# Optimization experiments

Measured on AMD Instinct MI355X. Metric: run time of the kernel, lower is better.

## Reference

```python
import jax, jax.numpy as jnp
import numpy as np

K = -1.0          # manifold curvature (hyperbolic / Poincare ball)
SK = 1.0          # sqrt(|K|)
EPS = 1e-7


def _artan_k(x):
    # inverse of tan_k for K<0: artanh(sqrt(|K|) x)/sqrt(|K|)
    return jnp.arctanh(jnp.clip(SK * x, -1.0 + EPS, 1.0 - EPS)) / SK


def _tan_k(x):
    return jnp.tanh(SK * x) / SK


def _norm(x):
    return jnp.maximum(jnp.linalg.norm(x, axis=-1, keepdims=True), 1e-15)


def mobius_add(x, y):
    xy = jnp.sum(x * y, -1, keepdims=True)
    x2 = jnp.sum(x * x, -1, keepdims=True)
    y2 = jnp.sum(y * y, -1, keepdims=True)
    num = (1.0 - 2.0 * K * xy - K * y2) * x + (1.0 + K * x2) * y
    den = 1.0 - 2.0 * K * xy + K * K * x2 * y2
    return num / jnp.maximum(den, 1e-15)


def mobius_scalar_mul(r, x):
    # r may be scalar or (n,1) per-row scalar
    xn = _norm(x)
    return _tan_k(r * _artan_k(xn)) * x / xn


def mobius_matvec(W, x):
    # geoopt convention: (m @ x) per point -> x @ W^T
    xn = _norm(x)
    mx = x @ W.T
    mxn = _norm(mx)
    return _tan_k(mxn / xn * _artan_k(xn)) * mx / mxn


def lambda_x(x):
    # conformal factor lambda_x = 2 / (1 + K |x|^2); returns shape (...,)
    return 2.0 / jnp.maximum(1.0 + K * jnp.sum(x * x, -1), 1e-10)


def expmap0(u):
    un = _norm(u)
    return _tan_k(un) * u / un


def logmap0(y):
    yn = _norm(y)
    return _artan_k(yn) * y / yn


def kappa_left_multiply(A, X):
    # Vectorized per-node weighted gyro-midpoint + mobius scalar mul.
    # out_i = (sum_j A_ij) otimes gyromidpoint(X, weights=A_i)
    gamma = lambda_x(X)                              # (n,)
    denom = A @ (gamma - 1.0)                        # (n,)
    denom = jnp.where(jnp.abs(denom) < 1e-10, 1e-10, denom)
    nom = A @ (gamma[:, None] * X)                   # (n,d)
    two_mean = nom / denom[:, None]
    m = mobius_scalar_mul(0.5, two_mean)             # gyromidpoint
    return mobius_scalar_mul(jnp.sum(A, axis=1, keepdims=True), m)


def setup_inputs() -> dict:
    key = jax.random.key(0)
    k1, k2, k3, k4, k5 = jax.random.split(key, 5)
    n, d, c = 8192, 256, 16
    # node embeddings on the Poincare ball (small norm, well inside the ball)
    X = 0.01 * jax.random.normal(k1, (n, d), jnp.float32)
    # dense normalized adjacency (positive weights, row sums O(1))
    A_hat = jax.random.uniform(k2, (n, n), dtype=jnp.float32) / n
    W = jax.random.uniform(k3, (d, d), dtype=jnp.float32)        # torch.rand init
    W_logits = jax.random.uniform(k4, (d, c), dtype=jnp.float32)
    # p_ks = expmap0(rand), scaled for numerical stability
    p_ks = expmap0(0.05 * jax.random.uniform(k5, (c, d), dtype=jnp.float32))
    return {"X": X, "A_hat": A_hat, "W": W, "W_logits": W_logits, "p_ks": p_ks}


def reference(X, A_hat, W, W_logits, p_ks):
    # hidden kappa-GCN layer
    XW = mobius_matvec(W, X)                          # (n,d)
    AXW = kappa_left_multiply(A_hat, XW)              # (n,d)
    H1 = expmap0(jax.nn.relu(logmap0(AXW)))           # manifold.apply(relu)
    # hyperbolic logits (kappa != 0 branch, K<0 -> asinh)
    z = mobius_add(-p_ks[None, :, :], H1[:, None, :]) # (n,k,d)
    z_n = jnp.linalg.norm(z, axis=-1)                 # (n,k)
    a_n = jnp.maximum(jnp.linalg.norm(W_logits, axis=0), 1e-15)  # (k,)
    za = jnp.einsum('nkd,dk->nk', z, W_logits)
    den = jnp.maximum(1.0 + K * z_n * z_n, 1e-10) * a_n
    dist = jnp.arcsinh(2.0 * SK * za / den)
    lam = lambda_x(p_ks)                              # (k,)
    logits = (lam * a_n / SK) * dist                  # (n,k)
    return A_hat @ logits
```

## Files before the change

kernel.cpp:

```cpp
#include <hip/hip_runtime.h>
#include <math.h>

#define Nn 8192
#define Dd 256
#define Cc 16

#define OFF_BP   4194304u
#define OFF_G1B  5373952u
#define OFF_DEN  5378048u
#define OFF_RS   5410816u
#define OFF_KC   5443584u
#define OFF_LB   5443648u
#define WS_FLOATS 5509184u

typedef short vshort8 __attribute__((ext_vector_type(8)));
typedef float vfloat4 __attribute__((ext_vector_type(4)));

#define AS1 __attribute__((address_space(1)))
#define AS3 __attribute__((address_space(3)))

__device__ __forceinline__ float clip1(float x) {
    return fminf(fmaxf(x, -1.0f + 1e-7f), 1.0f - 1e-7f);
}

__device__ __forceinline__ unsigned short f2bf(float f) {
    unsigned int u = __float_as_uint(f);
    u += 0x7fff + ((u >> 16) & 1);
    return (unsigned short)(u >> 16);
}

__device__ __forceinline__ float bf2f(unsigned short b) {
    return __uint_as_float(((unsigned int)b) << 16);
}

__device__ __forceinline__ float waveReduce(float v) {
    #pragma unroll
    for (int off = 32; off; off >>= 1) v += __shfl_down(v, off);
    return v;
}

__device__ __forceinline__ float blockReduceBcast(float v, float* red) {
    int t = threadIdx.x, w = t >> 6, l = t & 63;
    v = waveReduce(v);
    if (l == 0) red[w] = v;
    __syncthreads();
    if (t == 0) red[0] = red[0] + red[1] + red[2] + red[3];
    __syncthreads();
    float r = red[0];
    __syncthreads();
    return r;
}

__global__ __launch_bounds__(256) void k_front(const float* __restrict__ X,
                                               const float* __restrict__ W,
                                               const float* __restrict__ Wl,
                                               const float* __restrict__ Pk,
                                               unsigned short* __restrict__ Bp,
                                               unsigned short* __restrict__ g1b,
                                               float* __restrict__ kc) {
    __shared__ __align__(16) unsigned short Xs[32][256];
    __shared__ __align__(16) unsigned short Gs[32][258];
    __shared__ float xs2[32];
    __shared__ float scal[32];
    __shared__ float red4[32][4];

    const int t = threadIdx.x;

    if (blockIdx.x >= 256) {
        int k = blockIdx.x - 256;
        float* red = &red4[0][0];
        float pv = Pk[k * Dd + t];
        float wv = Wl[t * Cc + k];
        float p2 = blockReduceBcast(pv * pv, red);
        float pw = blockReduceBcast(pv * wv, red);
        float w2 = blockReduceBcast(wv * wv, red);
        if (t == 0) {
            float an  = fmaxf(sqrtf(w2), 1e-15f);
            float lam = 2.0f / fmaxf(1.0f - p2, 1e-10f);
            kc[k * 4 + 0] = p2; kc[k * 4 + 1] = pw;
            kc[k * 4 + 2] = an; kc[k * 4 + 3] = lam;
        }
        return;
    }

    const int l = t & 63, w = t >> 6;
    const int ll = l & 15, kh = l >> 4;
    const int m0 = blockIdx.x * 32;
    const int ar = t >> 3, aq = t & 7;
    const int c0 = w * 64;

    float x2p = 0.f;
    #pragma unroll
    for (int tc = 0; tc < 4; ++tc) {
        const float* xp = &X[(size_t)(m0 + ar) * Dd + tc * 64 + aq * 8];
        vfloat4 v0 = *(const vfloat4*)xp;
        vfloat4 v1 = *(const vfloat4*)(xp + 4);
        vshort8 o;
        #pragma unroll
        for (int e = 0; e < 4; ++e) {
            x2p += v0[e] * v0[e] + v1[e] * v1[e];
            o[e] = (short)f2bf(v0[e]);
            o[e + 4] = (short)f2bf(v1[e]);
        }
        int byte = (tc * 64 + aq * 8) * 2;
        *(vshort8*)((char*)&Xs[ar][0] + (byte ^ ((ar & 7) << 4))) = o;
    }
    x2p += __shfl_xor(x2p, 1); x2p += __shfl_xor(x2p, 2); x2p += __shfl_xor(x2p, 4);
    if (aq == 0) xs2[ar] = x2p;
    __syncthreads();

    vfloat4 acc[2][4];
    #pragma unroll
    for (int mi = 0; mi < 2; ++mi)
        #pragma unroll
        for (int ni = 0; ni < 4; ++ni)
            acc[mi][ni] = (vfloat4){0.f, 0.f, 0.f, 0.f};
    #pragma unroll
    for (int tc = 0; tc < 4; ++tc) {
        vshort8 bf[8];
        #pragma unroll
        for (int ni = 0; ni < 4; ++ni)
            #pragma unroll
            for (int kk = 0; kk < 2; ++kk) {
                const float* wp = &W[(size_t)(c0 + ni * 16 + ll) * Dd
                                     + tc * 64 + kh * 8 + kk * 32];
                vfloat4 b0 = *(const vfloat4*)wp;
                vfloat4 b1 = *(const vfloat4*)(wp + 4);
                vshort8 o;
                #pragma unroll
                for (int e = 0; e < 4; ++e) {
                    o[e] = (short)f2bf(b0[e]);
                    o[e + 4] = (short)f2bf(b1[e]);
                }
                bf[ni * 2 + kk] = o;
            }
        #pragma unroll
        for (int kk = 0; kk < 2; ++kk) {
            int byte = (tc * 64 + kh * 8 + kk * 32) * 2;
            vshort8 af[2];
            #pragma unroll
            for (int mi = 0; mi < 2; ++mi) {
                int row = mi * 16 + ll;
                af[mi] = *(const vshort8*)((const char*)&Xs[row][0]
                                           + (byte ^ ((row & 7) << 4)));
            }
            #pragma unroll
            for (int mi = 0; mi < 2; ++mi)
                #pragma unroll
                for (int ni = 0; ni < 4; ++ni)
                    acc[mi][ni] = __builtin_amdgcn_mfma_f32_16x16x32_bf16(
                        af[mi], bf[ni * 2 + kk], acc[mi][ni], 0, 0, 0);
        }
    }

    #pragma unroll
    for (int mi = 0; mi < 2; ++mi)
        #pragma unroll
        for (int j = 0; j < 4; ++j) {
            float p = 0.f;
            #pragma unroll
            for (int ni = 0; ni < 4; ++ni)
                p += acc[mi][ni][j] * acc[mi][ni][j];
            p += __shfl_xor(p, 1); p += __shfl_xor(p, 2);
            p += __shfl_xor(p, 4); p += __shfl_xor(p, 8);
            if (ll == 0) red4[mi * 16 + kh * 4 + j][w] = p;
        }
    __syncthreads();

    if (t < 32) {
        float mx2 = red4[t][0] + red4[t][1] + red4[t][2] + red4[t][3];
        float xn = fmaxf(sqrtf(xs2[t]), 1e-15f);
        float mxn = fmaxf(sqrtf(mx2), 1e-15f);
        float s = tanhf(mxn / xn * atanhf(clip1(xn))) / mxn;
        float xw2 = s * s * mx2;
        float gamma = 2.0f / fmaxf(1.0f - xw2, 1e-10f);
        scal[t] = gamma * s;
        g1b[m0 + t] = f2bf(gamma - 1.0f);
    }
    __syncthreads();

    #pragma unroll
    for (int mi = 0; mi < 2; ++mi)
        #pragma unroll
        for (int ni = 0; ni < 4; ++ni) {
            int row = mi * 16 + kh * 4;
            int col = c0 + ni * 16 + ll;
            #pragma unroll
            for (int j = 0; j < 4; ++j)
                Gs[row + j][col] = f2bf(scal[row + j] * acc[mi][ni][j]);
        }
    __syncthreads();

    const int s = blockIdx.x;
    #pragma unroll
    for (int pass = 0; pass < 4; ++pass) {
        int c = pass * 256 + t;
        int gni = c >> 6, lc = c & 63;
        int col = (gni >> 2) * 64 + (gni & 3) * 16 + (lc & 15);
        int kh8 = (lc >> 4) * 8;
        vshort8 o;
        #pragma unroll
        for (int e = 0; e < 8; ++e) o[e] = (short)Gs[kh8 + e][col];
        *(vshort8*)&Bp[((size_t)(s * 16 + gni) * 64 + lc) * 8] = o;
    }
}

__device__ __forceinline__ void g2_issueB(const unsigned short* __restrict__ Bp,
        unsigned short (&BsB)[16][512], int splt, int slab, int w, int l) {
    #pragma unroll
    for (int ni = 0; ni < 4; ++ni)
        __builtin_amdgcn_global_load_lds(
            (const AS1 unsigned int*)
                (Bp + ((size_t)((splt * 64 + slab) * 16 + w * 4 + ni) * 512) + l * 8),
            (AS3 unsigned int*)&BsB[w * 4 + ni][0], 16, 0, 0);
}

__device__ __forceinline__ void g2_loadA(const float* __restrict__ Abase,
                                         int tile, float (&a8)[8]) {
    const vfloat4* p = (const vfloat4*)(Abase + tile * 32);
    *(vfloat4*)&a8[0] = p[0];
    *(vfloat4*)&a8[4] = p[1];
}

__device__ __forceinline__ void g2_stage(unsigned short (&AsB)[2048],
        const unsigned short* g1s, const float (&a8)[8],
        int tile, int rowst, int kq, float& dacc, float& racc) {
    vshort8 gv = *(const vshort8*)&g1s[tile * 32 + kq * 8];
    vshort8 o;
    #pragma unroll
    for (int e = 0; e < 8; ++e) {
        float av = a8[e];
        o[e] = (short)f2bf(av);
        dacc += av * bf2f((unsigned short)gv[e]);
        racc += av;
    }
    *(vshort8*)((char*)&AsB[0] + rowst * 64 + ((kq * 16) ^ ((rowst & 3) << 4))) = o;
}

__device__ __forceinline__ void g2_mfma(const unsigned short (&AsB)[2048],
        const unsigned short (&BsB)[16][512], int w, int kh, int ll15, int l,
        vfloat4 (&acc)[4][4]) {
    vshort8 bf[4], af[4];
    #pragma unroll
    for (int ni = 0; ni < 4; ++ni)
        bf[ni] = *(const vshort8*)&BsB[w * 4 + ni][l * 8];
    #pragma unroll
    for (int mi = 0; mi < 4; ++mi) {
        int row = mi * 16 + ll15;
        af[mi] = *(const vshort8*)((const char*)&AsB[0]
                  + row * 64 + ((kh * 16) ^ ((row & 3) << 4)));
    }
    __builtin_amdgcn_s_setprio(1);
    #pragma unroll
    for (int mi = 0; mi < 4; ++mi)
        #pragma unroll
        for (int ni = 0; ni < 4; ++ni)
            acc[mi][ni] = __builtin_amdgcn_mfma_f32_16x16x32_bf16(
                af[mi], bf[ni], acc[mi][ni], 0, 0, 0);
    __builtin_amdgcn_s_setprio(0);
}

__global__ __launch_bounds__(256, 2) void k_gemm1_mfma(
        const float* __restrict__ A,
        const unsigned short* __restrict__ Bp,
        const unsigned short* __restrict__ g1b,
        unsigned short* __restrict__ Pp,
        float* __restrict__ denp,
        float* __restrict__ rsp) {
    __shared__ __align__(16) unsigned short As[2][2048];
    __shared__ __align__(16) unsigned short Bs[4][16][512];
    __shared__ __align__(16) unsigned short g1s[2048];

    const int t = threadIdx.x, l = t & 63, w = t >> 6;
    const int id = blockIdx.x;
    const int splt = id & 3;
    const int m0 = (id >> 2) * 64;
    const int kb = splt * 2048;
    const int kh = l >> 4, ll15 = l & 15;
    const int rowst = t >> 2, kq = t & 3;

    const float* Abase = &A[(size_t)(m0 + rowst) * Nn + kb + kq * 8];

    vfloat4 acc[4][4];
    #pragma unroll
    for (int mi = 0; mi < 4; ++mi)
        #pragma unroll
        for (int ni = 0; ni < 4; ++ni)
            acc[mi][ni] = (vfloat4){0.f, 0.f, 0.f, 0.f};
    float dacc = 0.f, racc = 0.f;
    float a0[8], a1[8], a2[8], a3[8];

    uint4 g1v = *(const uint4*)&g1b[kb + t * 8];
    g2_issueB(Bp, Bs[0], splt, 0, w, l);
    g2_issueB(Bp, Bs[1], splt, 1, w, l);
    g2_issueB(Bp, Bs[2], splt, 2, w, l);
    g2_loadA(Abase, 0, a0);
    g2_loadA(Abase, 1, a1);
    g2_loadA(Abase, 2, a2);
    g2_loadA(Abase, 3, a3);
    asm volatile("s_waitcnt vmcnt(0)" ::: "memory");
    *(uint4*)&g1s[t * 8] = g1v;
    asm volatile("s_waitcnt lgkmcnt(0)" ::: "memory");
    __builtin_amdgcn_s_barrier();
    g2_stage(As[0], g1s, a0, 0, rowst, kq, dacc, racc);
    asm volatile("s_waitcnt lgkmcnt(0)" ::: "memory");
    __builtin_amdgcn_s_barrier();
    __builtin_amdgcn_sched_barrier(0);

    for (int u = 0; u < 16; ++u) {
        #pragma unroll
        for (int pp = 0; pp < 4; ++pp) {
            const int q = u * 4 + pp;
            g2_issueB(Bp, Bs[(pp + 3) & 3], splt, (q + 3) & 63, w, l);
            {
                float (&adst)[8] = (pp == 0) ? a0 : (pp == 1) ? a1
                                 : (pp == 2) ? a2 : a3;
                g2_loadA(Abase, (q + 4) & 63, adst);
            }
            asm volatile("s_waitcnt vmcnt(18)" ::: "memory");
            if (q < 63) {
                float (&asrc)[8] = (pp == 0) ? a1 : (pp == 1) ? a2
                                 : (pp == 2) ? a3 : a0;
                g2_stage(As[(q + 1) & 1], g1s, asrc, q + 1, rowst, kq, dacc, racc);
            }
            g2_mfma(As[q & 1], Bs[pp & 3], w, kh, ll15, l, acc);
            asm volatile("s_waitcnt lgkmcnt(0)" ::: "memory");
            __builtin_amdgcn_s_barrier();
            __builtin_amdgcn_sched_barrier(0);
        }
    }

    dacc += __shfl_xor(dacc, 1); dacc += __shfl_xor(dacc, 2);
    racc += __shfl_xor(racc, 1); racc += __shfl_xor(racc, 2);
    if (kq == 0) {
        denp[splt * Nn + m0 + rowst] = dacc;
        rsp [splt * Nn + m0 + rowst] = racc;
    }

    unsigned short* P = Pp + (size_t)splt * ((size_t)Nn * Dd);
    #pragma unroll
    for (int mi = 0; mi < 4; ++mi)
        #pragma unroll
        for (int ni = 0; ni < 4; ++ni) {
            int row = m0 + mi * 16 + (kh << 2);
            int col = w * 64 + ni * 16 + ll15;
            #pragma unroll
            for (int j = 0; j < 4; ++j)
                P[(size_t)(row + j) * Dd + col] = f2bf(acc[mi][ni][j]);
        }
}

__global__ __launch_bounds__(256) void k_rowfix(const unsigned short* __restrict__ Pp,
                                                const float* __restrict__ denp,
                                                const float* __restrict__ rsp,
                                                const float* __restrict__ Pk,
                                                const float* __restrict__ Wl,
                                                const float* __restrict__ kc,
                                                unsigned short* __restrict__ Lb) {
    __shared__ float red[8];
    __shared__ float hs[256];
    __shared__ float PQ[16][2];
    int i = blockIdx.x, t = threadIdx.x;
    float nom = 0.f;
    #pragma unroll
    for (int s = 0; s < 4; ++s)
        nom += bf2f(Pp[(size_t)s * Nn * Dd + (size_t)i * Dd + t]);
    float dv = denp[i] + denp[Nn + i] + denp[2 * Nn + i] + denp[3 * Nn + i];
    dv = (fabsf(dv) < 1e-10f) ? 1e-10f : dv;
    float tm = nom / dv;
    float r2 = blockReduceBcast(tm * tm, red);
    float r = fmaxf(sqrtf(r2), 1e-15f);
    float mmul = tanhf(0.5f * atanhf(clip1(r))) / r;
    float mj = mmul * tm;
    float mn2 = blockReduceBcast(mj * mj, red);
    float mn = fmaxf(sqrtf(mn2), 1e-15f);
    float sA = rsp[i] + rsp[Nn + i] + rsp[2 * Nn + i] + rsp[3 * Nn + i];
    float axmul = tanhf(sA * atanhf(clip1(mn))) / mn;
    float axw = axmul * mj;
    float yn2 = blockReduceBcast(axw * axw, red);
    float yn = fmaxf(sqrtf(yn2), 1e-15f);
    float v = atanhf(clip1(yn)) / yn * axw;
    float u = fmaxf(v, 0.0f);
    float un2 = blockReduceBcast(u * u, red);
    float un = fmaxf(sqrtf(un2), 1e-15f);
    float h = tanhf(un) / un * u;
    float h2 = blockReduceBcast(h * h, red);
    hs[t] = h;
    __syncthreads();
    int w = t >> 6, l = t & 63;
    #pragma unroll
    for (int kk = 0; kk < 4; ++kk) {
        int k = w * 4 + kk;
        float pp = 0.f, qq = 0.f;
        #pragma unroll
        for (int m = 0; m < 4; ++m) {
            float hv = hs[l + 64 * m];
            pp += hv * Pk[k * Dd + l + 64 * m];
            qq += hv * Wl[(l + 64 * m) * Cc + k];
        }
        pp = waveReduce(pp);
        qq = waveReduce(qq);
        if (l == 0) { PQ[k][0] = pp; PQ[k][1] = qq; }
    }
    __syncthreads();
    if (t < 16) {
        int k = t;
        float p2 = kc[k * 4 + 0], pw = kc[k * 4 + 1];
        float an = kc[k * 4 + 2], lam = kc[k * 4 + 3];
        float P = PQ[k][0], Q = PQ[k][1];
        float alpha = 1.0f - 2.0f * P + h2;
        float beta  = 1.0f - p2;
        float Dm = fmaxf(1.0f - 2.0f * P + p2 * h2, 1e-15f);
        float za  = (-alpha * pw + beta * Q) / Dm;
        float zn2 = (alpha * alpha * p2 - 2.0f * alpha * beta * P + beta * beta * h2)
                    / (Dm * Dm);
        float dd = fmaxf(1.0f - zn2, 1e-10f) * an;
        float dist = asinhf(2.0f * za / dd);
        float lgv = lam * an * dist;
        int kt = i >> 5, r = i & 31;
        Lb[(size_t)kt * 512 + (size_t)(((r >> 3) * 16 + k) * 8) + (r & 7)]
            = f2bf(lgv);
    }
}

__global__ __launch_bounds__(256, 4) void k_gemm2_mfma(
        const float* __restrict__ A,
        const unsigned short* __restrict__ Lb,
        float* __restrict__ part) {
    const int t = threadIdx.x, l = t & 63, w = t >> 6;
    const int id = blockIdx.x;
    const int splt = id & 7;
    const int m0 = (id >> 3) * 64;
    const int kb = splt * 1024;
    const int kh = l >> 4, ll15 = l & 15;
    const int r0 = m0 + w * 16;

    const float* Ab = &A[(size_t)(r0 + ll15) * Nn + kb + kh * 8];
    const unsigned short* Lbb = &Lb[(size_t)(splt * 32) * 512 + l * 8];

    vfloat4 acc = (vfloat4){0.f, 0.f, 0.f, 0.f};
    float a0[8], a1[8], a2[8], a3[8];
    vshort8 b0, b1, b2, b3;

    *(vfloat4*)&a0[0] = *(const vfloat4*)(Ab);
    *(vfloat4*)&a0[4] = *(const vfloat4*)(Ab + 4);
    b0 = *(const vshort8*)(Lbb);
    *(vfloat4*)&a1[0] = *(const vfloat4*)(Ab + 32);
    *(vfloat4*)&a1[4] = *(const vfloat4*)(Ab + 36);
    b1 = *(const vshort8*)(Lbb + 512);
    *(vfloat4*)&a2[0] = *(const vfloat4*)(Ab + 64);
    *(vfloat4*)&a2[4] = *(const vfloat4*)(Ab + 68);
    b2 = *(const vshort8*)(Lbb + 1024);

    for (int u = 0; u < 8; ++u) {
        #pragma unroll
        for (int pp = 0; pp < 4; ++pp) {
            const int kt = u * 4 + pp;
            if (kt < 29) {
                float (&adst)[8] = (pp == 0) ? a3 : (pp == 1) ? a0
                                 : (pp == 2) ? a1 : a2;
                vshort8& bdst = (pp == 0) ? b3 : (pp == 1) ? b0
                              : (pp == 2) ? b1 : b2;
                *(vfloat4*)&adst[0] = *(const vfloat4*)(Ab + (kt + 3) * 32);
                *(vfloat4*)&adst[4] = *(const vfloat4*)(Ab + (kt + 3) * 32 + 4);
                bdst = *(const vshort8*)(Lbb + (kt + 3) * 512);
            }
            float (&acur)[8] = (pp == 0) ? a0 : (pp == 1) ? a1
                             : (pp == 2) ? a2 : a3;
            vshort8& bcur = (pp == 0) ? b0 : (pp == 1) ? b1
                          : (pp == 2) ? b2 : b3;
            vshort8 af;
            #pragma unroll
            for (int e = 0; e < 8; ++e) af[e] = (short)f2bf(acur[e]);
            acc = __builtin_amdgcn_mfma_f32_16x16x32_bf16(af, bcur, acc, 0, 0, 0);
        }
    }

    float* P = part + (size_t)splt * ((size_t)Nn * Cc);
    #pragma unroll
    for (int j = 0; j < 4; ++j)
        P[(size_t)(r0 + kh * 4 + j) * Cc + ll15] = acc[j];
}

__global__ __launch_bounds__(256) void k_reduce(const float* __restrict__ part,
                                                float* __restrict__ out) {
    int i = blockIdx.x * 256 + threadIdx.x;
    float s = 0.f;
    #pragma unroll
    for (int j = 0; j < 8; ++j) s += part[(size_t)j * (Nn * Cc) + i];
    out[i] = s;
}

extern "C" void kernel_launch(void* const* d_in, const int* in_sizes, int n_in,
                              void* d_out, int out_size, void* d_ws, size_t ws_size,
                              hipStream_t stream) {
    const float* X  = (const float*)d_in[0];
    const float* A  = (const float*)d_in[1];
    const float* W  = (const float*)d_in[2];
    const float* Wl = (const float*)d_in[3];
    const float* Pk = (const float*)d_in[4];
    float* out = (float*)d_out;
    float* ws = (float*)d_ws;
    if (ws_size < (size_t)WS_FLOATS * sizeof(float)) return;

    unsigned short* Pp  = (unsigned short*)ws;
    float* part = ws;
    unsigned short* Bp  = (unsigned short*)(ws + OFF_BP);
    unsigned short* g1b = (unsigned short*)(ws + OFF_G1B);
    float* denp = ws + OFF_DEN;
    float* rsp  = ws + OFF_RS;
    float* kc   = ws + OFF_KC;
    unsigned short* Lbp = (unsigned short*)(ws + OFF_LB);

    k_front<<<272, 256, 0, stream>>>(X, W, Wl, Pk, Bp, g1b, kc);
    k_gemm1_mfma<<<512, 256, 0, stream>>>(A, Bp, g1b, Pp, denp, rsp);
    k_rowfix<<<Nn, 256, 0, stream>>>(Pp, denp, rsp, Pk, Wl, kc, Lbp);
    k_gemm2_mfma<<<1024, 256, 0, stream>>>(A, Lbp, part);
    k_reduce<<<512, 256, 0, stream>>>(part, out);
}
```

Measured before the change: 204.3 us.

## Restructure GEMM1 pipeline to stage A in 4-tile groups with fewer barriers

The main GEMM loop now stages four A k-tiles at a time into a double-buffered group and synchronises the workgroup only once per group, instead of once per tile. B is double-buffered per wave with one tile of lookahead. Each wave loads and reads only its own B slice, so B needs no workgroup barrier. This cuts per-tile barrier and waitcnt stalls but shortens B prefetch depth and adds an explicit hand-written prologue and epilogue. That makes the vmcnt counts fragile.

```diff
diff --git a/kernel.cpp b/kernel.cpp
--- a/kernel.cpp
+++ b/kernel.cpp
@@ -222,7 +222,7 @@
     *(vfloat4*)&a8[4] = p[1];
 }
 
-__device__ __forceinline__ void g2_stage(unsigned short (&AsB)[2048],
+__device__ __forceinline__ void g2_stage(unsigned short (&AsT)[2048],
         const unsigned short* g1s, const float (&a8)[8],
         int tile, int rowst, int kq, float& dacc, float& racc) {
     vshort8 gv = *(const vshort8*)&g1s[tile * 32 + kq * 8];
@@ -234,10 +234,10 @@
         dacc += av * bf2f((unsigned short)gv[e]);
         racc += av;
     }
-    *(vshort8*)((char*)&AsB[0] + rowst * 64 + ((kq * 16) ^ ((rowst & 3) << 4))) = o;
-}
-
-__device__ __forceinline__ void g2_mfma(const unsigned short (&AsB)[2048],
+    *(vshort8*)((char*)&AsT[0] + rowst * 64 + ((kq * 16) ^ ((rowst & 3) << 4))) = o;
+}
+
+__device__ __forceinline__ void g2_mfma(const unsigned short (&AsT)[2048],
         const unsigned short (&BsB)[16][512], int w, int kh, int ll15, int l,
         vfloat4 (&acc)[4][4]) {
     vshort8 bf[4], af[4];
@@ -247,7 +247,7 @@
     #pragma unroll
     for (int mi = 0; mi < 4; ++mi) {
         int row = mi * 16 + ll15;
-        af[mi] = *(const vshort8*)((const char*)&AsB[0]
+        af[mi] = *(const vshort8*)((const char*)&AsT[0]
                   + row * 64 + ((kh * 16) ^ ((row & 3) << 4)));
     }
     __builtin_amdgcn_s_setprio(1);
@@ -267,8 +267,8 @@
         unsigned short* __restrict__ Pp,
         float* __restrict__ denp,
         float* __restrict__ rsp) {
-    __shared__ __align__(16) unsigned short As[2][2048];
-    __shared__ __align__(16) unsigned short Bs[4][16][512];
+    __shared__ __align__(16) unsigned short As[2][4][2048];
+    __shared__ __align__(16) unsigned short Bs[2][16][512];
     __shared__ __align__(16) unsigned short g1s[2048];
 
     const int t = threadIdx.x, l = t & 63, w = t >> 6;
@@ -288,47 +288,83 @@
         for (int ni = 0; ni < 4; ++ni)
             acc[mi][ni] = (vfloat4){0.f, 0.f, 0.f, 0.f};
     float dacc = 0.f, racc = 0.f;
-    float a0[8], a1[8], a2[8], a3[8];
-
-    uint4 g1v = *(const uint4*)&g1b[kb + t * 8];
-    g2_issueB(Bp, Bs[0], splt, 0, w, l);
-    g2_issueB(Bp, Bs[1], splt, 1, w, l);
-    g2_issueB(Bp, Bs[2], splt, 2, w, l);
-    g2_loadA(Abase, 0, a0);
-    g2_loadA(Abase, 1, a1);
-    g2_loadA(Abase, 2, a2);
-    g2_loadA(Abase, 3, a3);
+    float ar0[8], ar1[8];
+
+    {
+        uint4 g1v = *(const uint4*)&g1b[kb + t * 8];
+        g2_issueB(Bp, Bs[0], splt, 0, w, l);
+        float p0[8], p1[8], p2[8], p3[8];
+        g2_loadA(Abase, 0, p0);
+        g2_loadA(Abase, 1, p1);
+        g2_loadA(Abase, 2, p2);
+        g2_loadA(Abase, 3, p3);
+        g2_loadA(Abase, 4, ar1);
+        asm volatile("s_waitcnt vmcnt(0)" ::: "memory");
+        *(uint4*)&g1s[t * 8] = g1v;
+        g2_stage(As[0][0], g1s, p0, 0, rowst, kq, dacc, racc);
+        g2_stage(As[0][1], g1s, p1, 1, rowst, kq, dacc, racc);
+        g2_stage(As[0][2], g1s, p2, 2, rowst, kq, dacc, racc);
+        g2_stage(As[0][3], g1s, p3, 3, rowst, kq, dacc, racc);
+        asm volatile("s_waitcnt lgkmcnt(0)" ::: "memory");
+        __builtin_amdgcn_s_barrier();
+        __builtin_amdgcn_sched_barrier(0);
+    }
+
+    #pragma unroll 1
+    for (int v = 0; v < 7; ++v) {
+        #pragma unroll
+        for (int h = 0; h < 2; ++h) {
+            const int sp = v * 2 + h;
+            #pragma unroll
+            for (int pp = 0; pp < 4; ++pp) {
+                const int q = sp * 4 + pp;
+                g2_issueB(Bp, Bs[(pp + 1) & 1], splt, q + 1, w, l);
+                if (pp & 1) g2_loadA(Abase, q + 5, ar1);
+                else        g2_loadA(Abase, q + 5, ar0);
+                asm volatile("s_waitcnt vmcnt(6)" ::: "memory");
+                if (pp & 1) g2_stage(As[h ^ 1][pp], g1s, ar0, q + 4, rowst, kq, dacc, racc);
+                else        g2_stage(As[h ^ 1][pp], g1s, ar1, q + 4, rowst, kq, dacc, racc);
+                g2_mfma(As[h][pp], Bs[pp & 1], w, kh, ll15, l, acc);
+                if (pp == 3) {
+                    asm volatile("s_waitcnt lgkmcnt(0)" ::: "memory");
+                    __builtin_amdgcn_s_barrier();
+                    __builtin_amdgcn_sched_barrier(0);
+                }
+            }
+        }
+    }
+
+    #pragma unroll
+    for (int pp = 0; pp < 3; ++pp) {
+        const int q = 56 + pp;
+        g2_issueB(Bp, Bs[(pp + 1) & 1], splt, q + 1, w, l);
+        if (pp & 1) g2_loadA(Abase, q + 5, ar1);
+        else        g2_loadA(Abase, q + 5, ar0);
+        asm volatile("s_waitcnt vmcnt(6)" ::: "memory");
+        if (pp & 1) g2_stage(As[1][pp], g1s, ar0, q + 4, rowst, kq, dacc, racc);
+        else        g2_stage(As[1][pp], g1s, ar1, q + 4, rowst, kq, dacc, racc);
+        g2_mfma(As[0][pp], Bs[pp & 1], w, kh, ll15, l, acc);
+    }
+    {
+        g2_issueB(Bp, Bs[0], splt, 60, w, l);
+        asm volatile("s_waitcnt vmcnt(4)" ::: "memory");
+        g2_stage(As[1][3], g1s, ar0, 63, rowst, kq, dacc, racc);
+        g2_mfma(As[0][3], Bs[1], w, kh, ll15, l, acc);
+        asm volatile("s_waitcnt lgkmcnt(0)" ::: "memory");
+        __builtin_amdgcn_s_barrier();
+        __builtin_amdgcn_sched_barrier(0);
+    }
+    g2_issueB(Bp, Bs[1], splt, 61, w, l);
+    asm volatile("s_waitcnt vmcnt(4)" ::: "memory");
+    g2_mfma(As[1][0], Bs[0], w, kh, ll15, l, acc);
+    g2_issueB(Bp, Bs[0], splt, 62, w, l);
+    asm volatile("s_waitcnt vmcnt(4)" ::: "memory");
+    g2_mfma(As[1][1], Bs[1], w, kh, ll15, l, acc);
+    g2_issueB(Bp, Bs[1], splt, 63, w, l);
+    asm volatile("s_waitcnt vmcnt(4)" ::: "memory");
+    g2_mfma(As[1][2], Bs[0], w, kh, ll15, l, acc);
     asm volatile("s_waitcnt vmcnt(0)" ::: "memory");
-    *(uint4*)&g1s[t * 8] = g1v;
-    asm volatile("s_waitcnt lgkmcnt(0)" ::: "memory");
-    __builtin_amdgcn_s_barrier();
-    g2_stage(As[0], g1s, a0, 0, rowst, kq, dacc, racc);
-    asm volatile("s_waitcnt lgkmcnt(0)" ::: "memory");
-    __builtin_amdgcn_s_barrier();
-    __builtin_amdgcn_sched_barrier(0);
-
-    for (int u = 0; u < 16; ++u) {
-        #pragma unroll
-        for (int pp = 0; pp < 4; ++pp) {
-            const int q = u * 4 + pp;
-            g2_issueB(Bp, Bs[(pp + 3) & 3], splt, (q + 3) & 63, w, l);
-            {
-                float (&adst)[8] = (pp == 0) ? a0 : (pp == 1) ? a1
-                                 : (pp == 2) ? a2 : a3;
-                g2_loadA(Abase, (q + 4) & 63, adst);
-            }
-            asm volatile("s_waitcnt vmcnt(18)" ::: "memory");
-            if (q < 63) {
-                float (&asrc)[8] = (pp == 0) ? a1 : (pp == 1) ? a2
-                                 : (pp == 2) ? a3 : a0;
-                g2_stage(As[(q + 1) & 1], g1s, asrc, q + 1, rowst, kq, dacc, racc);
-            }
-            g2_mfma(As[q & 1], Bs[pp & 3], w, kh, ll15, l, acc);
-            asm volatile("s_waitcnt lgkmcnt(0)" ::: "memory");
-            __builtin_amdgcn_s_barrier();
-            __builtin_amdgcn_sched_barrier(0);
-        }
-    }
+    g2_mfma(As[1][3], Bs[1], w, kh, ll15, l, acc);
 
     dacc += __shfl_xor(dacc, 1); dacc += __shfl_xor(dacc, 2);
     racc += __shfl_xor(racc, 1); racc += __shfl_xor(racc, 2);
```

Measured after the change: 201.6 us. No clear change (-1.4%).
